# Performance work log

Measured on AMD Instinct MI355X. Metric: run time of the kernel, lower is better.

## Reference

```python
import jax, jax.numpy as jnp
import numpy as np
from math import factorial, pi

LMAX = 6      # max angular momentum
NMAX = 5      # max radial index
RC = 3.0      # PolyCut cutoff radius
UNIT = RC / 3.0

_one = np.ones((LMAX + 1, LMAX + 1), np.float32)
YR = jnp.asarray(2.0 * np.tril(_one) - np.eye(LMAX + 1, dtype=np.float32))
YI = jnp.asarray(2.0 * np.triu(_one, k=1))


def _nlm(l, m):
    return float(np.sqrt((2 * l + 1) / (4 * pi) * factorial(l - m) / factorial(l + m)))


def ylm_mat(v):
    """Solid harmonics r^l Y_lm for one point v=(x,y,z).
    Layout (as in AutoForce sph_repr): Re Y_l^m at [l, l-m]; Im Y_l^m at [l-m, l] for m>0,
    so YR (2*tril-eye) weights real parts (m=0 on the diagonal, weight 1) and
    YI (2*triu(1)) weights imaginary parts, reproducing the m-sum of the power spectrum."""
    x, y, z = v[0], v[1], v[2]
    r2 = x * x + y * y + z * z
    # (x + i y)^m by recursion
    A = [jnp.ones((), v.dtype)]
    B = [jnp.zeros((), v.dtype)]
    for m in range(1, LMAX + 1):
        A.append(x * A[m - 1] - y * B[m - 1])
        B.append(x * B[m - 1] + y * A[m - 1])
    # Pi_l^m(z, r^2): homogeneous associated-Legendre part of degree l-m
    Pi = {(0, 0): jnp.ones((), v.dtype)}
    for m in range(1, LMAX + 1):
        Pi[(m, m)] = (2 * m - 1) * Pi[(m - 1, m - 1)]  # (2m-1)!!
    for m in range(0, LMAX):
        Pi[(m + 1, m)] = (2 * m + 1) * z * Pi[(m, m)]
        for l in range(m + 2, LMAX + 1):
            Pi[(l, m)] = ((2 * l - 1) * z * Pi[(l - 1, m)]
                          - (l + m - 1) * r2 * Pi[(l - 2, m)]) / (l - m)
    Y = jnp.zeros((LMAX + 1, LMAX + 1), v.dtype)
    for l in range(LMAX + 1):
        for m in range(l + 1):
            cnl = _nlm(l, m)
            Y = Y.at[l, l - m].set(cnl * Pi[(l, m)] * A[m])
            if m > 0:
                Y = Y.at[l - m, l].set(cnl * Pi[(l, m)] * B[m])
    return Y


def radial(dist):
    # PolyCut: (1 - d/rc)^2 inside rc, and its derivative
    step = (dist < RC).astype(dist.dtype)
    t = 1.0 - dist / RC
    return step * t * t, -2.0 * step * t / RC


def setup_inputs() -> dict:
    key = jax.random.key(0)
    coo = jax.random.normal(key, (150000, 3), dtype=jnp.float32)
    return {"coo": coo}


def reference(coo):
    xyz = coo / UNIT                                   # (N, 3)
    d = jnp.sqrt(jnp.sum(xyz * xyz, axis=-1))          # (N,)
    n = 2.0 * jnp.arange(NMAX + 1, dtype=coo.dtype)    # even powers 0,2,...,2*nmax
    r, dr = radial(UNIT * d)
    dr = UNIT * dr
    f = r[None] * d[None] ** n[:, None]                # (nmax+1, N)
    Y = jnp.transpose(jax.vmap(ylm_mat)(xyz), (1, 2, 0))                   # (L+1, L+1, N)
    dY = jnp.transpose(jax.vmap(jax.jacfwd(ylm_mat))(xyz), (1, 2, 0, 3))   # (L+1, L+1, N, 3)
    c = jnp.einsum('nj,lmj->nlm', f, Y)                # (nmax+1, L+1, L+1)
    # p[i,k,l] = sum_m YR[l,m]*c[i,l,m]*c[k,l,m] + sum_m YI[m,l]*c[i,m,l]*c[k,m,l]
    p = (jnp.einsum('ilm,klm,lm->ikl', c, c, YR)
         + jnp.einsum('iml,kml,ml->ikl', c, c, YI))    # (nmax+1, nmax+1, L+1)
    # hand-derived gradient chain, as in the torch module
    df = dr[None] * d[None] ** n[:, None] + r[None] * n[:, None] * d[None] ** (n[:, None] - 1.0)
    dfv = df[..., None] * xyz / d[:, None]             # (nmax+1, N, 3)
    dc = (dfv[:, None, None] * Y[None, ..., None]
          + f[:, None, None, :, None] * dY[None])      # (nmax+1, L+1, L+1, N, 3)
    # dp without materializing dnnp: contract dc with (c*YR) / (c*YI) directly
    cYr = c * YR
    cYi = c * YI
    dp = (jnp.einsum('klm,ilmjx->ikljx', cYr, dc)
          + jnp.einsum('ilm,klmjx->ikljx', cYr, dc)
          + jnp.einsum('kml,imljx->ikljx', cYi, dc)
          + jnp.einsum('iml,kmljx->ikljx', cYi, dc))   # (nmax+1, nmax+1, L+1, N, 3)
    return p, dp / UNIT
```

## Files before the change

### kernel.cpp

```cpp
#include <hip/hip_runtime.h>


#define LMAXV 6
#define NSZ 6
#define RCV 3.0f

typedef float float3v __attribute__((ext_vector_type(3)));

__device__ __forceinline__ int xcd_chunk(int b, int nblk) {
    const int q = nblk >> 3, rr = nblk & 7;
    const int xcd = b & 7, idx = b >> 3;
    return (xcd < rr ? xcd * (q + 1) : rr * (q + 1) + (xcd - rr) * q) + idx;
}

constexpr double csqrt_(double x) {
    double y = x > 1.0 ? x : 1.0;
    for (int i = 0; i < 100; ++i) y = 0.5 * (y + x / y);
    return y;
}
constexpr double factd_(int n) { double r = 1.0; for (int i = 2; i <= n; ++i) r *= i; return r; }
constexpr double PI_D = 3.14159265358979323846;
struct CnlT { float v[7][7]; };
constexpr CnlT make_cnl_() {
    CnlT t{};
    for (int l = 0; l <= 6; ++l)
        for (int m = 0; m <= 6; ++m)
            t.v[l][m] = (m <= l)
                ? (float)csqrt_((2.0 * l + 1.0) / (4.0 * PI_D) * factd_(l - m) / factd_(l + m))
                : 0.0f;
    return t;
}
__device__ constexpr CnlT CNL = make_cnl_();
__device__ constexpr float DFACT[7] = {1.f, 1.f, 3.f, 15.f, 105.f, 945.f, 10395.f};

__global__ void k_zero(float* __restrict__ cws) {
    int t = blockIdx.x * blockDim.x + threadIdx.x;
    if (t < NSZ * 49) cws[t] = 0.0f;
}

__global__ __launch_bounds__(256) void k_creduce(const float* __restrict__ coo,
                                                 float* __restrict__ cws, int N) {
    const int i_rad = blockIdx.y;
    float acc[7][7];
#pragma unroll
    for (int a = 0; a < 7; ++a)
#pragma unroll
        for (int b = 0; b < 7; ++b) acc[a][b] = 0.0f;

    const int stride = gridDim.x * blockDim.x;
    for (int j = blockIdx.x * blockDim.x + threadIdx.x; j < N; j += stride) {
        float x = coo[3 * j + 0], y = coo[3 * j + 1], z = coo[3 * j + 2];
        float r2 = x * x + y * y + z * z;
        float dn = sqrtf(r2);
        float tt = 1.0f - dn * (1.0f / RCV);
        float r  = (dn < RCV) ? tt * tt : 0.0f;
        float fi = r;
        for (int q = 0; q < i_rad; ++q) fi *= r2;

        float Av[7], Bv[7];
        Av[0] = 1.0f; Bv[0] = 0.0f;
#pragma unroll
        for (int m = 1; m <= 6; ++m) {
            Av[m] = x * Av[m - 1] - y * Bv[m - 1];
            Bv[m] = x * Bv[m - 1] + y * Av[m - 1];
        }

        float P1[7], P2[7];
#pragma unroll
        for (int l = 0; l <= 6; ++l) {
            float PC[7];
#pragma unroll
            for (int mm = 0; mm <= l; ++mm) {
                float pv;
                if (mm == l)            pv = DFACT[l];
                else if (mm == l - 1)   pv = (float)(2 * l - 1) * z * P1[mm];
                else {
                    float a = (float)(2 * l - 1), b = (float)(l + mm - 1);
                    pv = (a * z * P1[mm] - b * r2 * P2[mm]) * (1.0f / (float)(l - mm));
                }
                PC[mm] = pv;
                float base = fi * CNL.v[l][mm] * pv;
                acc[l][l - mm] += base * Av[mm];
                if (mm >= 1) acc[l - mm][l] += base * Bv[mm];
            }
#pragma unroll
            for (int mm = 0; mm <= l; ++mm) { P2[mm] = P1[mm]; P1[mm] = PC[mm]; }
        }
    }

    __shared__ float sblk[49];
    if (threadIdx.x < 49) sblk[threadIdx.x] = 0.0f;
    __syncthreads();
    const int lane = threadIdx.x & 63;
#pragma unroll
    for (int a = 0; a < 7; ++a)
#pragma unroll
        for (int b = 0; b < 7; ++b) {
            float v = acc[a][b];
            v += __shfl_down(v, 32);
            v += __shfl_down(v, 16);
            v += __shfl_down(v, 8);
            v += __shfl_down(v, 4);
            v += __shfl_down(v, 2);
            v += __shfl_down(v, 1);
            if (lane == 0) atomicAdd(&sblk[a * 7 + b], v);
        }
    __syncthreads();
    if (threadIdx.x < 49) atomicAdd(&cws[i_rad * 49 + threadIdx.x], sblk[threadIdx.x]);
}

__global__ void k_p(const float* __restrict__ cws, float* __restrict__ out) {
    int t = threadIdx.x;
    if (t >= 252) return;
    int i = t / 42, k = (t / 7) % 6, l = t % 7;
    const float* ci = cws + i * 49;
    const float* ck = cws + k * 49;
    float s = 0.0f;
    for (int mm = 0; mm <= l; ++mm) {
        float w = (mm == 0) ? 1.0f : 2.0f;
        s += w * ci[l * 7 + (l - mm)] * ck[l * 7 + (l - mm)];
        if (mm >= 1) s += 2.0f * ci[(l - mm) * 7 + l] * ck[(l - mm) * 7 + l];
    }
    out[t] = s;
}

__global__ __launch_bounds__(256) void k_dp(const float* __restrict__ coo,
                                            const float* __restrict__ cws,
                                            float* __restrict__ out, int N,
                                            int nblk) {
    __shared__ float sRe[7][7][6];
    __shared__ float sIm[7][7][6];
    for (int s = threadIdx.x; s < 294; s += blockDim.x) {
        int k = s % 6; int lm = s / 6; int l = lm / 7; int mm = lm % 7;
        float re = 0.0f, im = 0.0f;
        if (mm <= l)            re = ((mm == 0) ? 1.0f : 2.0f) * cws[k * 49 + l * 7 + (l - mm)];
        if (mm >= 1 && mm <= l) im = 2.0f * cws[k * 49 + (l - mm) * 7 + l];
        sRe[l][mm][k] = re;
        sIm[l][mm][k] = im;
    }
    __syncthreads();

    const int chunk = xcd_chunk(blockIdx.x, nblk);
    const int j0 = chunk * 256;
    const int jglob = j0 + (int)threadIdx.x;
    const bool active = jglob < N;
    const int jj = active ? jglob : (N - 1);

    const float x = coo[3 * jj + 0], y = coo[3 * jj + 1], z = coo[3 * jj + 2];
    const float r2 = x * x + y * y + z * z;
    const float dn = sqrtf(r2);
    const float invd = 1.0f / dn;
    const float inv2r2 = 0.5f / r2;

    float Av[7], Bv[7];
    Av[0] = 1.0f; Bv[0] = 0.0f;
#pragma unroll
    for (int m = 1; m <= 6; ++m) {
        Av[m] = x * Av[m - 1] - y * Bv[m - 1];
        Bv[m] = x * Bv[m - 1] + y * Av[m - 1];
    }

    float S[7][NSZ], TX[7][NSZ], TY[7][NSZ];
#pragma unroll
    for (int l = 0; l < 7; ++l)
#pragma unroll
        for (int k = 0; k < NSZ; ++k) { S[l][k] = 0.f; TX[l][k] = 0.f; TY[l][k] = 0.f; }

    {
        float P1v[7], P1z[7], P2v[7], P2z[7];
#pragma unroll
        for (int mm = 0; mm < 7; ++mm) { P1v[mm] = 0.f; P1z[mm] = 0.f; P2v[mm] = 0.f; P2z[mm] = 0.f; }

#pragma unroll
        for (int l = 0; l <= LMAXV; ++l) {
            const float lf  = (float)l;
            const float a2l = 2.0f * lf - 1.0f;
#pragma unroll
            for (int mm = 0; mm <= 6; ++mm) {
                if (mm <= l) {
                    const float b  = lf + (float)(mm - 1);
                    const float ic = (l > mm) ? (1.0f / (float)(l - mm)) : 1.0f;
                    float pv = (a2l * z * P1v[mm] - b * r2 * P2v[mm]) * ic;
                    float pz = (a2l * (P1v[mm] + z * P1z[mm]) - b * r2 * P2z[mm]) * ic;
                    if (mm == l) pv = DFACT[l];
                    const float pr = ((lf - (float)mm) * pv - z * pz) * inv2r2;
                    P2v[mm] = P1v[mm]; P2z[mm] = P1z[mm];
                    P1v[mm] = pv; P1z[mm] = pz;

                    const float c0  = CNL.v[l][mm];
                    const float cp  = c0 * pv;
                    const float prx = c0 * 2.0f * pr;
                    const float pmv = cp * (float)mm;
                    const int  mp  = (mm > 0) ? mm - 1 : 0;

                    const float ReV = cp * Av[mm];
                    const float ReX = prx * x * Av[mm] + pmv * Av[mp];
                    const float ReG = prx * y * Av[mm] - pmv * Bv[mp];
#pragma unroll
                    for (int k = 0; k < NSZ; ++k) {
                        const float cc = sRe[l][mm][k];
                        S[l][k]  += cc * ReV;
                        TX[l][k] += cc * ReX;
                        TY[l][k] += cc * ReG;
                    }
                    if (mm >= 1) {
                        const float ImV = cp * Bv[mm];
                        const float ImX = prx * x * Bv[mm] + pmv * Bv[mp];
                        const float ImG = prx * y * Bv[mm] + pmv * Av[mp];
#pragma unroll
                        for (int k = 0; k < NSZ; ++k) {
                            const float cc = sIm[l][mm][k];
                            S[l][k]  += cc * ImV;
                            TX[l][k] += cc * ImX;
                            TY[l][k] += cc * ImG;
                        }
                    }
                }
            }
        }
    }

    const float tt = 1.0f - dn * (1.0f / RCV);
    const bool  ins = dn < RCV;
    const float r  = ins ? tt * tt : 0.0f;
    const float dr = ins ? (-2.0f / RCV) * tt : 0.0f;
    const float ux = x * invd, uy = y * invd, uz = z * invd;
    const float zs = (fabsf(z) < 1e-20f) ? 1e-20f : z;
    const float invz = 1.0f / zs;
    float f[NSZ], dfi[NSZ];
    {
        float p2 = 1.0f;
#pragma unroll
        for (int i = 0; i < NSZ; ++i) {
            f[i] = r * p2;
            dfi[i] = p2 * (dr + (float)(2 * i) * r * invd);
            p2 *= r2;
        }
    }

    if (!active) return;

    const uint32_t sliceB = (uint32_t)N * 12u;
    char* const outB = (char*)out;
    uint32_t off = 1008u + (uint32_t)jglob * 12u;
#pragma unroll
    for (int ik = 0; ik < 36; ++ik) {
        const int i = ik / 6, k = ik % 6;
        const int a = (i < k) ? i : k;
        const int c = (i < k) ? k : i;
#pragma unroll
        for (int l = 0; l < 7; ++l) {
            const float gg = dfi[a] * S[l][c] + dfi[c] * S[l][a];
            const float sf = f[a] * S[l][c] + f[c] * S[l][a];
            const float fx = f[a] * TX[l][c] + f[c] * TX[l][a];
            const float fy = f[a] * TY[l][c] + f[c] * TY[l][a];
            const float fz = ((float)l * sf - x * fx - y * fy) * invz;
            float3v v;
            v.x = ux * gg + fx;
            v.y = uy * gg + fy;
            v.z = uz * gg + fz;
            *(float3v*)(outB + off) = v;
            off += sliceB;
        }
    }
}

extern "C" void kernel_launch(void* const* d_in, const int* in_sizes, int n_in,
                              void* d_out, int out_size, void* d_ws, size_t ws_size,
                              hipStream_t stream) {
    const float* coo = (const float*)d_in[0];
    float* out = (float*)d_out;
    float* cws = (float*)d_ws;
    const int N = in_sizes[0] / 3;
    const int nb = (N + 255) / 256;

    hipLaunchKernelGGL(k_zero, dim3(1), dim3(320), 0, stream, cws);
    hipLaunchKernelGGL(k_creduce, dim3(128, 6), dim3(256), 0, stream, coo, cws, N);
    hipLaunchKernelGGL(k_p, dim3(1), dim3(256), 0, stream, cws, out);
    hipLaunchKernelGGL(k_dp, dim3(nb), dim3(256), 0, stream, coo, cws, out, N, nb);
}
```

Baseline: 159.6 us.

## Stage per-point S/TX/TY partials in LDS to cut register pressure in k_dp

Moves the 126 per-point accumulators (S, TX, TY for each l and radial index) out of registers into a per-thread LDS staging array, filled one l at a time. The output loop becomes non-unrolled and recomputes f and df per (a,c) pair from powers of r2 instead of holding them in arrays. Coefficients are now read straight from global/constant-cached cws rather than a shared table, and the block size drops to 128 threads. The aim is lower VGPR use and higher occupancy for the store-bound write phase, at the cost of many LDS reads and writes, uncoalesced scalar loads of cws, and extra multiplies in the rolled loop.

```diff
diff --git a/kernel.cpp b/kernel.cpp
--- a/kernel.cpp
+++ b/kernel.cpp
@@ -4,6 +4,7 @@
 #define LMAXV 6
 #define NSZ 6
 #define RCV 3.0f
+#define TPB 128
 
 typedef float float3v __attribute__((ext_vector_type(3)));
 
@@ -124,27 +125,17 @@
     out[t] = s;
 }
 
-__global__ __launch_bounds__(256) void k_dp(const float* __restrict__ coo,
+__global__ __launch_bounds__(TPB) void k_dp(const float* __restrict__ coo,
                                             const float* __restrict__ cws,
                                             float* __restrict__ out, int N,
                                             int nblk) {
-    __shared__ float sRe[7][7][6];
-    __shared__ float sIm[7][7][6];
-    for (int s = threadIdx.x; s < 294; s += blockDim.x) {
-        int k = s % 6; int lm = s / 6; int l = lm / 7; int mm = lm % 7;
-        float re = 0.0f, im = 0.0f;
-        if (mm <= l)            re = ((mm == 0) ? 1.0f : 2.0f) * cws[k * 49 + l * 7 + (l - mm)];
-        if (mm >= 1 && mm <= l) im = 2.0f * cws[k * 49 + (l - mm) * 7 + l];
-        sRe[l][mm][k] = re;
-        sIm[l][mm][k] = im;
-    }
-    __syncthreads();
+    __shared__ float stage[126][TPB];
 
     const int chunk = xcd_chunk(blockIdx.x, nblk);
-    const int j0 = chunk * 256;
-    const int jglob = j0 + (int)threadIdx.x;
+    const int jglob = chunk * TPB + (int)threadIdx.x;
     const bool active = jglob < N;
     const int jj = active ? jglob : (N - 1);
+    const int tid = (int)threadIdx.x;
 
     const float x = coo[3 * jj + 0], y = coo[3 * jj + 1], z = coo[3 * jj + 2];
     const float r2 = x * x + y * y + z * z;
@@ -160,12 +151,6 @@
         Bv[m] = x * Bv[m - 1] + y * Av[m - 1];
     }
 
-    float S[7][NSZ], TX[7][NSZ], TY[7][NSZ];
-#pragma unroll
-    for (int l = 0; l < 7; ++l)
-#pragma unroll
-        for (int k = 0; k < NSZ; ++k) { S[l][k] = 0.f; TX[l][k] = 0.f; TY[l][k] = 0.f; }
-
     {
         float P1v[7], P1z[7], P2v[7], P2z[7];
 #pragma unroll
@@ -175,6 +160,10 @@
         for (int l = 0; l <= LMAXV; ++l) {
             const float lf  = (float)l;
             const float a2l = 2.0f * lf - 1.0f;
+            float Sl[NSZ], TXl[NSZ], TYl[NSZ];
+#pragma unroll
+            for (int k = 0; k < NSZ; ++k) { Sl[k] = 0.f; TXl[k] = 0.f; TYl[k] = 0.f; }
+
 #pragma unroll
             for (int mm = 0; mm <= 6; ++mm) {
                 if (mm <= l) {
@@ -196,12 +185,13 @@
                     const float ReV = cp * Av[mm];
                     const float ReX = prx * x * Av[mm] + pmv * Av[mp];
                     const float ReG = prx * y * Av[mm] - pmv * Bv[mp];
+                    const float w0 = (mm == 0) ? 1.0f : 2.0f;
 #pragma unroll
                     for (int k = 0; k < NSZ; ++k) {
-                        const float cc = sRe[l][mm][k];
-                        S[l][k]  += cc * ReV;
-                        TX[l][k] += cc * ReX;
-                        TY[l][k] += cc * ReG;
+                        const float cc = w0 * cws[k * 49 + l * 7 + (l - mm)];
+                        Sl[k]  += cc * ReV;
+                        TXl[k] += cc * ReX;
+                        TYl[k] += cc * ReG;
                     }
                     if (mm >= 1) {
                         const float ImV = cp * Bv[mm];
@@ -209,13 +199,19 @@
                         const float ImG = prx * y * Bv[mm] + pmv * Av[mp];
 #pragma unroll
                         for (int k = 0; k < NSZ; ++k) {
-                            const float cc = sIm[l][mm][k];
-                            S[l][k]  += cc * ImV;
-                            TX[l][k] += cc * ImX;
-                            TY[l][k] += cc * ImG;
+                            const float ci = 2.0f * cws[k * 49 + (l - mm) * 7 + l];
+                            Sl[k]  += ci * ImV;
+                            TXl[k] += ci * ImX;
+                            TYl[k] += ci * ImG;
                         }
                     }
                 }
+            }
+#pragma unroll
+            for (int k = 0; k < NSZ; ++k) {
+                stage[0 * 42 + l * 6 + k][tid] = Sl[k];
+                stage[1 * 42 + l * 6 + k][tid] = TXl[k];
+                stage[2 * 42 + l * 6 + k][tid] = TYl[k];
             }
         }
     }
@@ -227,33 +223,34 @@
     const float ux = x * invd, uy = y * invd, uz = z * invd;
     const float zs = (fabsf(z) < 1e-20f) ? 1e-20f : z;
     const float invz = 1.0f / zs;
-    float f[NSZ], dfi[NSZ];
-    {
-        float p2 = 1.0f;
-#pragma unroll
-        for (int i = 0; i < NSZ; ++i) {
-            f[i] = r * p2;
-            dfi[i] = p2 * (dr + (float)(2 * i) * r * invd);
-            p2 *= r2;
-        }
-    }
 
     if (!active) return;
 
     const uint32_t sliceB = (uint32_t)N * 12u;
     char* const outB = (char*)out;
     uint32_t off = 1008u + (uint32_t)jglob * 12u;
-#pragma unroll
+    int ii = 0, kk = 0;
+#pragma unroll 1
     for (int ik = 0; ik < 36; ++ik) {
-        const int i = ik / 6, k = ik % 6;
-        const int a = (i < k) ? i : k;
-        const int c = (i < k) ? k : i;
+        const int a = (ii < kk) ? ii : kk;
+        const int c = (ii < kk) ? kk : ii;
+        float p2a = 1.0f; for (int q = 0; q < a; ++q) p2a *= r2;
+        float p2c = 1.0f; for (int q = 0; q < c; ++q) p2c *= r2;
+        const float fa = r * p2a, fc = r * p2c;
+        const float da = p2a * (dr + (float)(2 * a) * r * invd);
+        const float dc = p2c * (dr + (float)(2 * c) * r * invd);
 #pragma unroll
         for (int l = 0; l < 7; ++l) {
-            const float gg = dfi[a] * S[l][c] + dfi[c] * S[l][a];
-            const float sf = f[a] * S[l][c] + f[c] * S[l][a];
-            const float fx = f[a] * TX[l][c] + f[c] * TX[l][a];
-            const float fy = f[a] * TY[l][c] + f[c] * TY[l][a];
+            const float Sa  = stage[l * 6 + a][tid];
+            const float Sc  = stage[l * 6 + c][tid];
+            const float TXa = stage[42 + l * 6 + a][tid];
+            const float TXc = stage[42 + l * 6 + c][tid];
+            const float TYa = stage[84 + l * 6 + a][tid];
+            const float TYc = stage[84 + l * 6 + c][tid];
+            const float gg = da * Sc + dc * Sa;
+            const float sf = fa * Sc + fc * Sa;
+            const float fx = fa * TXc + fc * TXa;
+            const float fy = fa * TYc + fc * TYa;
             const float fz = ((float)l * sf - x * fx - y * fy) * invz;
             float3v v;
             v.x = ux * gg + fx;
@@ -262,6 +259,7 @@
             *(float3v*)(outB + off) = v;
             off += sliceB;
         }
+        if (++kk == 6) { kk = 0; ++ii; }
     }
 }
 
@@ -272,10 +270,10 @@
     float* out = (float*)d_out;
     float* cws = (float*)d_ws;
     const int N = in_sizes[0] / 3;
-    const int nb = (N + 255) / 256;
+    const int nb = (N + TPB - 1) / TPB;
 
     hipLaunchKernelGGL(k_zero, dim3(1), dim3(320), 0, stream, cws);
     hipLaunchKernelGGL(k_creduce, dim3(128, 6), dim3(256), 0, stream, coo, cws, N);
     hipLaunchKernelGGL(k_p, dim3(1), dim3(256), 0, stream, cws, out);
-    hipLaunchKernelGGL(k_dp, dim3(nb), dim3(256), 0, stream, coo, cws, out, N, nb);
-}
+    hipLaunchKernelGGL(k_dp, dim3(nb), dim3(TPB), 0, stream, coo, cws, out, N, nb);
+}
```

Measured after the change: 154.4 us. 1.03x faster.
